# Kernel optimization log

Measured on AMD Instinct MI355X. Metric: run time of the kernel, lower is better.

Reference implementation:

```python
import jax, jax.numpy as jnp
import numpy as np

RES = 256
DEC = 8
NUM_MEAS = RES * RES // DEC  # 8192
BATCH = 4


def _bilinear_gather(img, coords):
    """grid_sample-style bilinear interpolation (align_corners=True, zero padding).
    img: [B, C, H, W]; coords: [M, 2] with (x, y) in pixel-centered units [-res/2, res/2].
    Returns [B, C, M]."""
    B, C, H, W = img.shape
    # normalize to [-1, 1] then map to pixel index space (align_corners=True)
    gx = (coords[:, 0] / (W / 2) + 1.0) * 0.5 * (W - 1)
    gy = (coords[:, 1] / (H / 2) + 1.0) * 0.5 * (H - 1)
    x0 = jnp.floor(gx)
    y0 = jnp.floor(gy)
    wx1 = gx - x0
    wx0 = 1.0 - wx1
    wy1 = gy - y0
    wy0 = 1.0 - wy1
    x0i = x0.astype(jnp.int32)
    y0i = y0.astype(jnp.int32)

    def tap(xi, yi, w):
        valid = ((xi >= 0) & (xi < W) & (yi >= 0) & (yi < H)).astype(img.dtype)
        xc = jnp.clip(xi, 0, W - 1)
        yc = jnp.clip(yi, 0, H - 1)
        v = img[:, :, yc, xc]  # [B, C, M] advanced-index gather
        return v * (w * valid)[None, None, :]

    return (tap(x0i, y0i, wx0 * wy0) + tap(x0i + 1, y0i, wx1 * wy0)
            + tap(x0i, y0i + 1, wx0 * wy1) + tap(x0i + 1, y0i + 1, wx1 * wy1))


def _nufft_adjoint(s, coords, N):
    """Exact adjoint non-uniform DFT (the math the gridding NUFFT approximates).
    s: [B, M] complex samples at k-space locations coords [M, 2] (pixel units, centered).
    out[b, y, x] = sum_m s[b,m] * exp(2j*pi*(kx_m*(x-N/2) + ky_m*(y-N/2))/N)."""
    n = jnp.arange(N, dtype=jnp.float32) - N / 2  # centered image coords
    two_pi = jnp.float32(2.0 * np.pi)
    Ex = jnp.exp(1j * (two_pi * coords[:, 0:1] * n[None, :] / N)).astype(jnp.complex64)  # [M, N]
    Ey = jnp.exp(1j * (two_pi * coords[:, 1:2] * n[None, :] / N)).astype(jnp.complex64)  # [M, N]
    t = s[:, :, None] * Ey[None, :, :]          # [B, M, H]
    return jnp.einsum('bmy,mx->byx', t, Ex)     # [B, H, W] complex64


def setup_inputs() -> dict:
    key = jax.random.key(0)
    k1, k2 = jax.random.split(key)
    inp = jax.random.normal(k1, (BATCH, 1, RES, RES, 2), dtype=jnp.float32)
    # gaussian trajectory init: randn * res / 6 (learnable parameter)
    x = jax.random.normal(k2, (NUM_MEAS, 2), dtype=jnp.float32) * (RES / 6.0)
    return {"input": inp, "x": x}


def reference(input, x):
    # [B,1,H,W,2] -> [B,2,H,W] (real/imag as channels)
    img = jnp.transpose(input, (0, 1, 4, 2, 3))[:, 0]
    B, C, H, W = img.shape
    sub_ksp = _bilinear_gather(img, x)                      # [B, 2, M]
    s = (sub_ksp[:, 0] + 1j * sub_ksp[:, 1]).astype(jnp.complex64)  # [B, M]
    out_c = _nufft_adjoint(s, x, H)                          # [B, H, W]
    out = jnp.stack([out_c.real, out_c.imag], axis=-1)       # [B, H, W, 2]
    return out[:, None]                                      # [B, 1, H, W, 2]
```

## Files before the change

### kernel.cpp

```cpp
#include <hip/hip_runtime.h>
#include <hip/hip_bf16.h>
#include <stdint.h>
#include <math.h>

#define RES     256
#define M_MEAS  8192
#define BATCH   4
#define KDIM    8192
#define ROWS    2048
#define NCOLS   288
#define SINOFF  144
#define SPLIT   16
#define KCHUNK  512
#define BM      128
#define BN      96
#define BK      32
#define NT      (KCHUNK / BK)

typedef __attribute__((ext_vector_type(8))) __bf16 bf16x8;
typedef __attribute__((ext_vector_type(8))) unsigned short u16x8;
typedef __attribute__((ext_vector_type(4))) float f32x4;
typedef __attribute__((ext_vector_type(2))) float f32x2;

#define OFF_A  262144
#define OFF_B  33816576
#define OFF_C  38535168

__device__ __forceinline__ unsigned short f2bf(float f) {
    unsigned u = __float_as_uint(f);
    u += 0x7FFFu + ((u >> 16) & 1u);
    return (unsigned short)(u >> 16);
}

__device__ __forceinline__ void lds_load16(const void* g, void* l) {
    __builtin_amdgcn_global_load_lds(
        (const __attribute__((address_space(1))) uint32_t*)(uintptr_t)g,
        (__attribute__((address_space(3))) uint32_t*)(uint32_t)(uintptr_t)l,
        16, 0, 0);
}

__global__ __launch_bounds__(256) void k_gather(const float* __restrict__ in,
                                                const float* __restrict__ xs,
                                                float* __restrict__ sRe,
                                                float* __restrict__ sIm) {
    int t = blockIdx.x * 256 + threadIdx.x;
    int b = t >> 13, m = t & (M_MEAS - 1);
    float kx = xs[2 * m + 0], ky = xs[2 * m + 1];
    float gx = (kx * (1.0f / 128.0f) + 1.0f) * 0.5f * 255.0f;
    float gy = (ky * (1.0f / 128.0f) + 1.0f) * 0.5f * 255.0f;
    float fx0 = floorf(gx), fy0 = floorf(gy);
    float wx1 = gx - fx0, wx0 = 1.0f - wx1;
    float wy1 = gy - fy0, wy0 = 1.0f - wy1;
    int x0 = (int)fx0, y0 = (int)fy0;
    float re = 0.0f, im = 0.0f;
#pragma unroll
    for (int dy = 0; dy < 2; ++dy) {
#pragma unroll
        for (int dx = 0; dx < 2; ++dx) {
            int xi = x0 + dx, yi = y0 + dy;
            bool v = (xi >= 0) && (xi < RES) && (yi >= 0) && (yi < RES);
            int xc = min(max(xi, 0), RES - 1);
            int yc = min(max(yi, 0), RES - 1);
            float w = (dx ? wx1 : wx0) * (dy ? wy1 : wy0) * (v ? 1.0f : 0.0f);
            const float* p = in + ((((size_t)b * RES + yc) * RES + xc) * 2);
            re += p[0] * w;
            im += p[1] * w;
        }
    }
    sRe[b * M_MEAS + m] = re;
    sIm[b * M_MEAS + m] = im;
}

__global__ __launch_bounds__(256) void k_buildAB(const float* __restrict__ xs,
                                                 const float* __restrict__ sRe,
                                                 const float* __restrict__ sIm,
                                                 unsigned short* __restrict__ A,
                                                 unsigned short* __restrict__ Bt) {
    int blk = blockIdx.x;
    if (blk < 1024) {
        int t = blk * 256 + threadIdx.x;
        int y  = t >> 10;
        int m0 = (t & 1023) * 8;
        float n = (float)(y - 128);
        float c[8], s_[8];
#pragma unroll
        for (int j = 0; j < 8; ++j) {
            float ky = xs[2 * (m0 + j) + 1];
            float u = ky * n * (1.0f / 256.0f);
            u -= rintf(u);
            float th = u * 6.28318530717958647692f;
            s_[j] = __sinf(th);
            c[j]  = __cosf(th);
        }
#pragma unroll
        for (int b = 0; b < BATCH; ++b) {
            u16x8 vr, vi;
#pragma unroll
            for (int j = 0; j < 8; ++j) {
                float sr = sRe[b * M_MEAS + m0 + j];
                float si = sIm[b * M_MEAS + m0 + j];
                vr[j] = f2bf(sr * c[j] - si * s_[j]);
                vi[j] = f2bf(sr * s_[j] + si * c[j]);
            }
            *(u16x8*)(A + ((size_t)b * 512 + y) * KDIM + m0)       = vr;
            *(u16x8*)(A + ((size_t)b * 512 + 256 + y) * KDIM + m0) = vi;
        }
    } else {
        int t = (blk - 1024) * 256 + threadIdx.x;
        int cidx = t >> 10;
        int m0 = (t & 1023) * 8;
        bool isCos = cidx < SINOFF;
        int u = isCos ? cidx : (cidx - SINOFF);
        u16x8 v;
        if (u > 128) {
            v = (u16x8){0, 0, 0, 0, 0, 0, 0, 0};
        } else {
            float nn = (float)u;
#pragma unroll
            for (int j = 0; j < 8; ++j) {
                float kx = xs[2 * (m0 + j) + 0];
                float ur = kx * nn * (1.0f / 256.0f);
                ur -= rintf(ur);
                float th = ur * 6.28318530717958647692f;
                v[j] = f2bf(isCos ? __cosf(th) : __sinf(th));
            }
        }
        *(u16x8*)(Bt + (size_t)cidx * KDIM + m0) = v;
    }
}

__global__ __launch_bounds__(256) void k_gemm(const unsigned short* __restrict__ A,
                                              const unsigned short* __restrict__ Bt,
                                              float* __restrict__ Cp) {
    __shared__ __align__(16) unsigned short As[2][BM * BK];
    __shared__ __align__(16) unsigned short Bs[2][BN * BK];

    int bid   = blockIdx.x;
    int tile  = bid >> 4;
    int split = bid & 15;
    int tr = tile / 3, tc = tile - tr * 3;
    int row0 = tr * BM, col0 = tc * BN;
    int kbase = split * KCHUNK;
    int tid = threadIdx.x;
    int w = tid >> 6, l = tid & 63;
    int wr = w >> 1, wc = w & 1;

    int srow = tid >> 2;
    int skoff = (tid & 3) * 8;

    f32x4 acc[4][3] = {};
    int lr = l & 15, lk = (l >> 4) * 8;

#define STAGE(buf, k0)                                                          \
    do {                                                                        \
        lds_load16(A + (size_t)(row0 + srow) * KDIM + (k0) + skoff,             \
                   &As[buf][(size_t)tid * 8]);                                  \
        lds_load16(A + (size_t)(row0 + 64 + srow) * KDIM + (k0) + skoff,        \
                   &As[buf][(size_t)(256 + tid) * 8]);                          \
        lds_load16(Bt + (size_t)(col0 + srow) * KDIM + (k0) + skoff,            \
                   &Bs[buf][(size_t)tid * 8]);                                  \
        if (tid < 128)                                                          \
            lds_load16(Bt + (size_t)(col0 + 64 + srow) * KDIM + (k0) + skoff,   \
                       &Bs[buf][(size_t)(256 + tid) * 8]);                      \
    } while (0)

    STAGE(0, kbase);
    __syncthreads();

    int cur = 0;
    for (int kt = 0; kt < NT; ++kt) {
        if (kt < NT - 1) STAGE(cur ^ 1, kbase + (kt + 1) * BK);

        bf16x8 af[4], bfr[3];
#pragma unroll
        for (int i = 0; i < 4; ++i)
            af[i]  = *(const bf16x8*)(&As[cur][(wr * 64 + i * 16 + lr) * BK + lk]);
#pragma unroll
        for (int j = 0; j < 3; ++j)
            bfr[j] = *(const bf16x8*)(&Bs[cur][(wc * 48 + j * 16 + lr) * BK + lk]);
#pragma unroll
        for (int i = 0; i < 4; ++i)
#pragma unroll
            for (int j = 0; j < 3; ++j)
                acc[i][j] = __builtin_amdgcn_mfma_f32_16x16x32_bf16(af[i], bfr[j], acc[i][j], 0, 0, 0);

        __syncthreads();
        cur ^= 1;
    }
#undef STAGE

    float* Cb = Cp + (size_t)split * ROWS * NCOLS;
#pragma unroll
    for (int i = 0; i < 4; ++i) {
#pragma unroll
        for (int j = 0; j < 3; ++j) {
            int colg = col0 + wc * 48 + j * 16 + (l & 15);
#pragma unroll
            for (int v = 0; v < 4; ++v) {
                int rowg = row0 + wr * 64 + i * 16 + (l >> 4) * 4 + v;
                Cb[(size_t)rowg * NCOLS + colg] = acc[i][j][v];
            }
        }
    }
}

__global__ __launch_bounds__(256) void k_combine(const float* __restrict__ Cp,
                                                 float* __restrict__ out) {
    int t = blockIdx.x * 256 + threadIdx.x;
    int x = t & 255, y = (t >> 8) & 255, b = t >> 16;
    int n = x - 128;
    int u = (n < 0) ? -n : n;
    float sg = (n < 0) ? -1.0f : 1.0f;
    size_t rRe = ((size_t)b * 512 + y) * NCOLS;
    size_t rIm = rRe + (size_t)256 * NCOLS;
    float cr = 0.0f, sr = 0.0f, ci = 0.0f, si = 0.0f;
#pragma unroll
    for (int s2 = 0; s2 < SPLIT; ++s2) {
        const float* Cb = Cp + (size_t)s2 * ROWS * NCOLS;
        cr += Cb[rRe + u];
        sr += Cb[rRe + SINOFF + u];
        ci += Cb[rIm + u];
        si += Cb[rIm + SINOFF + u];
    }
    float re = cr - sg * si;
    float im = sg * sr + ci;
    ((f32x2*)out)[t] = (f32x2){re, im};
}

extern "C" void kernel_launch(void* const* d_in, const int* in_sizes, int n_in,
                              void* d_out, int out_size, void* d_ws, size_t ws_size,
                              hipStream_t stream) {
    const float* in = (const float*)d_in[0];
    const float* xs = (const float*)d_in[1];
    float* out = (float*)d_out;
    char* ws = (char*)d_ws;

    float* sRe = (float*)ws;
    float* sIm = sRe + BATCH * M_MEAS;
    unsigned short* A  = (unsigned short*)(ws + OFF_A);
    unsigned short* Bt = (unsigned short*)(ws + OFF_B);
    float* Cp = (float*)(ws + OFF_C);

    k_gather <<<128,         256, 0, stream>>>(in, xs, sRe, sIm);
    k_buildAB<<<1024 + 1152, 256, 0, stream>>>(xs, sRe, sIm, A, Bt);
    k_gemm   <<<768,         256, 0, stream>>>(A, Bt, Cp);
    k_combine<<<1024,        256, 0, stream>>>(Cp, out);
}
```

Before: 50.09 us.

## Deepen GEMM K-tile, swizzle LDS layout, and restructure the prefetch pipeline

The split-K GEMM now uses a 64-wide K tile with an XOR-swizzled LDS layout meant to avoid bank conflicts on the fragment reads. The main loop is fully unrolled and keeps two stages in flight: it waits with explicit vmcnt counts, loads all fragments into registers, then issues the next global-to-LDS stage before running the MFMAs, so loads overlap compute. Launch bounds request two blocks per CU. The cost is twice the LDS per block, more fragment registers, and hand-placed waitcnt and barrier timing that depends on how lds_load16 is implemented.

Result: faster. 48.59 us (-3.0%).

```diff
diff --git a/kernel.cpp b/kernel.cpp
--- a/kernel.cpp
+++ b/kernel.cpp
@@ -14,7 +14,7 @@
 #define KCHUNK  512
 #define BM      128
 #define BN      96
-#define BK      32
+#define BK      64
 #define NT      (KCHUNK / BK)
 
 typedef __attribute__((ext_vector_type(8))) __bf16 bf16x8;
@@ -129,9 +129,9 @@
     }
 }
 
-__global__ __launch_bounds__(256) void k_gemm(const unsigned short* __restrict__ A,
-                                              const unsigned short* __restrict__ Bt,
-                                              float* __restrict__ Cp) {
+__global__ __launch_bounds__(256, 2) void k_gemm(const unsigned short* __restrict__ A,
+                                                 const unsigned short* __restrict__ Bt,
+                                                 float* __restrict__ Cp) {
     __shared__ __align__(16) unsigned short As[2][BM * BK];
     __shared__ __align__(16) unsigned short Bs[2][BN * BK];
 
@@ -145,47 +145,68 @@
     int w = tid >> 6, l = tid & 63;
     int wr = w >> 1, wc = w & 1;
 
-    int srow = tid >> 2;
-    int skoff = (tid & 3) * 8;
-
     f32x4 acc[4][3] = {};
-    int lr = l & 15, lk = (l >> 4) * 8;
-
-#define STAGE(buf, k0)                                                          \
-    do {                                                                        \
-        lds_load16(A + (size_t)(row0 + srow) * KDIM + (k0) + skoff,             \
-                   &As[buf][(size_t)tid * 8]);                                  \
-        lds_load16(A + (size_t)(row0 + 64 + srow) * KDIM + (k0) + skoff,        \
-                   &As[buf][(size_t)(256 + tid) * 8]);                          \
-        lds_load16(Bt + (size_t)(col0 + srow) * KDIM + (k0) + skoff,            \
-                   &Bs[buf][(size_t)tid * 8]);                                  \
-        if (tid < 128)                                                          \
-            lds_load16(Bt + (size_t)(col0 + 64 + srow) * KDIM + (k0) + skoff,   \
-                       &Bs[buf][(size_t)(256 + tid) * 8]);                      \
+    int lr = l & 15, lu = l >> 4;
+
+#define STAGE(buf, k0)                                                            \
+    do {                                                                          \
+        _Pragma("unroll")                                                         \
+        for (int q = 0; q < 4; ++q) {                                             \
+            int U = q * 256 + tid;                                                \
+            int r = U >> 3, u = U & 7;                                            \
+            lds_load16(A + (size_t)(row0 + r) * KDIM + (k0) + ((u ^ (r & 7)) * 8),\
+                       &As[buf][(size_t)U * 8]);                                  \
+        }                                                                         \
+        _Pragma("unroll")                                                         \
+        for (int q = 0; q < 3; ++q) {                                             \
+            int U = q * 256 + tid;                                                \
+            int r = U >> 3, u = U & 7;                                            \
+            lds_load16(Bt + (size_t)(col0 + r) * KDIM + (k0) + ((u ^ (r & 7)) * 8),\
+                       &Bs[buf][(size_t)U * 8]);                                  \
+        }                                                                         \
     } while (0)
 
     STAGE(0, kbase);
-    __syncthreads();
-
-    int cur = 0;
-    for (int kt = 0; kt < NT; ++kt) {
-        if (kt < NT - 1) STAGE(cur ^ 1, kbase + (kt + 1) * BK);
-
-        bf16x8 af[4], bfr[3];
-#pragma unroll
-        for (int i = 0; i < 4; ++i)
-            af[i]  = *(const bf16x8*)(&As[cur][(wr * 64 + i * 16 + lr) * BK + lk]);
-#pragma unroll
-        for (int j = 0; j < 3; ++j)
-            bfr[j] = *(const bf16x8*)(&Bs[cur][(wc * 48 + j * 16 + lr) * BK + lk]);
-#pragma unroll
-        for (int i = 0; i < 4; ++i)
-#pragma unroll
-            for (int j = 0; j < 3; ++j)
-                acc[i][j] = __builtin_amdgcn_mfma_f32_16x16x32_bf16(af[i], bfr[j], acc[i][j], 0, 0, 0);
-
-        __syncthreads();
-        cur ^= 1;
+    STAGE(1, kbase + BK);
+
+#pragma unroll
+    for (int t = 0; t < NT; ++t) {
+        int cur = t & 1;
+        if (t < NT - 1) asm volatile("s_waitcnt vmcnt(7)" ::: "memory");
+        else            asm volatile("s_waitcnt vmcnt(0)" ::: "memory");
+        __builtin_amdgcn_sched_barrier(0);
+        __builtin_amdgcn_s_barrier();
+        __builtin_amdgcn_sched_barrier(0);
+
+        bf16x8 af[2][4], bfr[2][3];
+#pragma unroll
+        for (int ks = 0; ks < 2; ++ks) {
+#pragma unroll
+            for (int i = 0; i < 4; ++i) {
+                int row = wr * 64 + i * 16 + lr;
+                af[ks][i] = *(const bf16x8*)(&As[cur][row * 64 + (((ks << 2) | lu) ^ (row & 7)) * 8]);
+            }
+#pragma unroll
+            for (int j = 0; j < 3; ++j) {
+                int row = wc * 48 + j * 16 + lr;
+                bfr[ks][j] = *(const bf16x8*)(&Bs[cur][row * 64 + (((ks << 2) | lu) ^ (row & 7)) * 8]);
+            }
+        }
+        __builtin_amdgcn_sched_barrier(0);
+        asm volatile("s_waitcnt lgkmcnt(0)" ::: "memory");
+        __builtin_amdgcn_sched_barrier(0);
+        __builtin_amdgcn_s_barrier();
+        __builtin_amdgcn_sched_barrier(0);
+
+        if (t < NT - 2) STAGE(cur, kbase + (t + 2) * BK);
+
+#pragma unroll
+        for (int ks = 0; ks < 2; ++ks)
+#pragma unroll
+            for (int i = 0; i < 4; ++i)
+#pragma unroll
+                for (int j = 0; j < 3; ++j)
+                    acc[i][j] = __builtin_amdgcn_mfma_f32_16x16x32_bf16(af[ks][i], bfr[ks][j], acc[i][j], 0, 0, 0);
     }
 #undef STAGE
 
```
